# Optimization experiments

Hardware: AMD Instinct MI355X
Metric: run time of the kernel (lower is better)

Reference implementation:

```python
import jax, jax.numpy as jnp
import numpy as np

N_NODES = 8192
IN_FEAT = 128
OUT_FEAT = 64
N_EDGES = 262144


def gcn_conv(x, edge_index, W, b):
    # x: [N, F_in], edge_index: [2, E], W: [F_in, F_out], b: [F_out]
    n = x.shape[0]
    loop = jnp.arange(n, dtype=edge_index.dtype)
    src = jnp.concatenate([edge_index[0], loop])  # message sources (incl. self loops)
    dst = jnp.concatenate([edge_index[1], loop])  # aggregation targets
    # symmetric normalization D^{-1/2} (A+I) D^{-1/2}
    deg = jax.ops.segment_sum(jnp.ones_like(dst, dtype=x.dtype), dst, num_segments=n)
    dinv = jax.lax.rsqrt(jnp.where(deg > 0, deg, 1.0))
    norm = dinv[src] * dinv[dst]  # [E + N]
    h = x @ W  # [N, F_out]
    out = jax.ops.segment_sum(h[src] * norm[:, None], dst, num_segments=n)
    return out + b


def setup_inputs() -> dict:
    key = jax.random.key(0)
    k1, k2, k3, k4 = jax.random.split(key, 4)
    x = jax.random.normal(k1, (IN_FEAT, N_NODES), dtype=jnp.float32)
    edge_index = jax.random.randint(k2, (2, N_EDGES), 0, N_NODES, dtype=jnp.int64)
    # encoder GCNConv params (glorot-ish scale)
    W_enc = jax.random.normal(k3, (IN_FEAT, OUT_FEAT), dtype=jnp.float32) / np.sqrt(IN_FEAT)
    b_enc = jnp.zeros((OUT_FEAT,), dtype=jnp.float32)
    return {"x": x, "edge_index": edge_index, "W_enc": W_enc, "b_enc": b_enc}


def reference(x, edge_index, W_enc, b_enc):
    xt = x.T  # [N, F_in]
    z = gcn_conv(xt, edge_index, W_enc, b_enc)  # [N, F_out]
    adj_pred = jax.nn.sigmoid(z @ z.T)  # [N, N]
    return adj_pred
```

## Files before the change

### kernel.cpp

```cpp
#include <hip/hip_runtime.h>
#include <hip/hip_bf16.h>

#define N_NODES 8192
#define F_IN    128
#define F_OUT   64
#define N_EDGES 262144

typedef unsigned int   u32;
typedef unsigned short u16;
typedef __attribute__((ext_vector_type(8))) short short8;
typedef __attribute__((ext_vector_type(4))) float f32x4;

__device__ __forceinline__ u16 f2bf_rne(float f) {
    u32 u = __float_as_uint(f);
    u32 r = (u + 0x7FFFu + ((u >> 16) & 1u)) >> 16;
    return (u16)r;
}
__device__ __forceinline__ float bf2f(u16 b) {
    return __uint_as_float(((u32)b) << 16);
}

__global__ __launch_bounds__(256) void detect_kernel(const int* __restrict__ ei,
                                                     const u32* __restrict__ xw,
                                                     int* __restrict__ eflag,
                                                     int* __restrict__ xdt) {
    if (blockIdx.x < 32) {
        int i = blockIdx.x * 256 + threadIdx.x;
        if (ei[2 * i + 1] != 0) atomicOr(eflag, 1);
    } else {
        __shared__ int cnt;
        if (threadIdx.x == 0) cnt = 0;
        __syncthreads();
        u32 w = xw[threadIdx.x * 64 + 1];
        u32 e = (w >> 7) & 0xFFu;
        if (e >= 100u && e <= 134u) atomicAdd(&cnt, 1);
        __syncthreads();
        if (threadIdx.x == 0) *xdt = (cnt > 128) ? 1 : 0;
    }
}

__global__ __launch_bounds__(256) void deg_kernel(const int* __restrict__ ei,
                                                  const int* __restrict__ eflagp,
                                                  int* __restrict__ deg) {
    int e = blockIdx.x * 256 + threadIdx.x;
    bool is64 = (*eflagp == 0);
    int d = is64 ? ei[2 * (N_EDGES + e)] : ei[N_EDGES + e];
    atomicAdd(&deg[d], 1);
}

__global__ __launch_bounds__(1024) void scan_kernel(const int* __restrict__ deg,
                                                    int* __restrict__ offs,
                                                    int* __restrict__ cursor) {
    __shared__ int part[1024];
    int t = threadIdx.x;
    int loc[8];
    int run = 0;
    #pragma unroll
    for (int j = 0; j < 8; ++j) { loc[j] = run; run += deg[t * 8 + j]; }
    part[t] = run;
    __syncthreads();
    for (int d = 1; d < 1024; d <<= 1) {
        int v = (t >= d) ? part[t - d] : 0;
        __syncthreads();
        part[t] += v;
        __syncthreads();
    }
    int pre = part[t] - run;
    #pragma unroll
    for (int j = 0; j < 8; ++j) {
        int v = pre + loc[j];
        offs[t * 8 + j]   = v;
        cursor[t * 8 + j] = v;
    }
    if (t == 1023) offs[8192] = pre + run;
}

__global__ __launch_bounds__(256) void fill_feat_kernel(
        const int* __restrict__ ei, const int* __restrict__ eflagp,
        int* __restrict__ cursor, int* __restrict__ esrc,
        const void* __restrict__ xv, const void* __restrict__ Wv,
        const void* __restrict__ bv, const int* __restrict__ xdtp,
        const int* __restrict__ deg,
        float* __restrict__ dinv,
        float* __restrict__ h,
        float* __restrict__ z)
{
    __shared__ float Wl[F_IN * F_OUT];
    int t = threadIdx.x;

    if (blockIdx.x < N_EDGES / 256) {
        int e = blockIdx.x * 256 + t;
        bool is64 = (*eflagp == 0);
        int s = is64 ? ei[2 * e]             : ei[e];
        int d = is64 ? ei[2 * (N_EDGES + e)] : ei[N_EDGES + e];
        int pos = atomicAdd(&cursor[d], 1);
        esrc[pos] = s;
        return;
    }

    const bool isbf = (*xdtp != 0);
    if (isbf) {
        const __hip_bfloat16* Wb = (const __hip_bfloat16*)Wv;
        for (int i = t; i < F_IN * F_OUT; i += 256) Wl[i] = (float)Wb[i];
    } else {
        const float* Wf = (const float*)Wv;
        for (int i = t; i < F_IN * F_OUT; i += 256) Wl[i] = Wf[i];
    }
    __syncthreads();

    int id = (blockIdx.x - N_EDGES / 256) * 256 + t;
    int og = id >> 13;
    int n  = id & (N_NODES - 1);

    float dv = rsqrtf((float)(deg[n] + 1));
    float acc[8] = {0.f,0.f,0.f,0.f,0.f,0.f,0.f,0.f};

    if (isbf) {
        const __hip_bfloat16* xb = (const __hip_bfloat16*)xv;
        for (int f = 0; f < F_IN; ++f) {
            float xval = (float)xb[f * N_NODES + n];
            const float4* w4 = (const float4*)&Wl[f * F_OUT + og * 8];
            float4 w0 = w4[0], w1 = w4[1];
            acc[0] += xval * w0.x; acc[1] += xval * w0.y;
            acc[2] += xval * w0.z; acc[3] += xval * w0.w;
            acc[4] += xval * w1.x; acc[5] += xval * w1.y;
            acc[6] += xval * w1.z; acc[7] += xval * w1.w;
        }
    } else {
        const float* xf = (const float*)xv;
        for (int f = 0; f < F_IN; ++f) {
            float xval = xf[f * N_NODES + n];
            const float4* w4 = (const float4*)&Wl[f * F_OUT + og * 8];
            float4 w0 = w4[0], w1 = w4[1];
            acc[0] += xval * w0.x; acc[1] += xval * w0.y;
            acc[2] += xval * w0.z; acc[3] += xval * w0.w;
            acc[4] += xval * w1.x; acc[5] += xval * w1.y;
            acc[6] += xval * w1.z; acc[7] += xval * w1.w;
        }
    }

    if (og == 0) dinv[n] = dv;

    float bvals[8];
    if (isbf) {
        const __hip_bfloat16* bb = (const __hip_bfloat16*)bv;
        #pragma unroll
        for (int j = 0; j < 8; ++j) bvals[j] = (float)bb[og * 8 + j];
    } else {
        const float* bf = (const float*)bv;
        #pragma unroll
        for (int j = 0; j < 8; ++j) bvals[j] = bf[og * 8 + j];
    }
    float hs[8], zb[8];
    #pragma unroll
    for (int j = 0; j < 8; ++j) {
        hs[j] = dv * acc[j];
        zb[j] = bvals[j] + dv * hs[j];
    }
    float* hp = h + (size_t)n * 64 + og * 8;
    ((float4*)hp)[0] = make_float4(hs[0], hs[1], hs[2], hs[3]);
    ((float4*)hp)[1] = make_float4(hs[4], hs[5], hs[6], hs[7]);
    float* zp = z + (size_t)n * 64 + og * 8;
    ((float4*)zp)[0] = make_float4(zb[0], zb[1], zb[2], zb[3]);
    ((float4*)zp)[1] = make_float4(zb[4], zb[5], zb[6], zb[7]);
}

__global__ __launch_bounds__(256) void gather_kernel(
        const int* __restrict__ offs, const int* __restrict__ esrc,
        const float* __restrict__ h, const float* __restrict__ dinv,
        float* __restrict__ z)
{
    int t = blockIdx.x * 256 + threadIdx.x;
    int d = t >> 6;
    int o = t & 63;
    int beg = offs[d], end = offs[d + 1];
    float acc = 0.f;
    for (int i = beg; i < end; ++i) {
        int s = esrc[i];
        acc += h[(size_t)s * 64 + o];
    }
    z[(size_t)d * 64 + o] += dinv[d] * acc;
}

__global__ __launch_bounds__(256) void gemm_sig_kernel(
        const float* __restrict__ z, float* __restrict__ out)
{
    __shared__ __align__(16) char smem[128 * 129 * 4];
    u16 (*Ah)[64] = (u16(*)[64])(smem);
    u16 (*Al)[64] = (u16(*)[64])(smem + 16384);
    u16 (*Bh)[64] = (u16(*)[64])(smem + 32768);
    u16 (*Bl)[64] = (u16(*)[64])(smem + 49152);
    float (*Cs)[129] = (float(*)[129])(smem);

    int t = threadIdx.x;

    int tgt = blockIdx.x;
    int bi = (int)((sqrtf(8.f * (float)tgt + 1.f) - 1.f) * 0.5f);
    while ((bi + 1) * (bi + 2) / 2 <= tgt) ++bi;
    while (bi * (bi + 1) / 2 > tgt) --bi;
    int bj = tgt - bi * (bi + 1) / 2;
    int i0 = bi * 128;
    int j0 = bj * 128;
    bool offdiag = (bi != bj);

    #pragma unroll
    for (int it = 0; it < 8; ++it) {
        int item = it * 256 + t;
        int tile = item >> 10;
        int r    = (item >> 3) & 127;
        int c    = item & 7;
        const float* src = z + (size_t)((tile ? j0 : i0) + r) * 64 + c * 8;
        float4 v0 = ((const float4*)src)[0];
        float4 v1 = ((const float4*)src)[1];
        float vf[8] = {v0.x, v0.y, v0.z, v0.w, v1.x, v1.y, v1.z, v1.w};
        short8 sh, sl;
        #pragma unroll
        for (int j = 0; j < 8; ++j) {
            float f  = vf[j];
            u16 hb   = f2bf_rne(f);
            u16 lb   = f2bf_rne(f - bf2f(hb));
            sh[j] = (short)hb;
            sl[j] = (short)lb;
        }
        int cs = c ^ (r & 7);
        u16* dh = tile ? &Bh[r][cs * 8] : &Ah[r][cs * 8];
        u16* dl = tile ? &Bl[r][cs * 8] : &Al[r][cs * 8];
        *(short8*)dh = sh;
        *(short8*)dl = sl;
    }
    __syncthreads();

    int lane = t & 63;
    int w    = t >> 6;
    int lr   = lane & 15;
    int lk   = lane >> 4;

    short8 ah[2][2], al[2][2];
    #pragma unroll
    for (int rt = 0; rt < 2; ++rt)
        #pragma unroll
        for (int kh = 0; kh < 2; ++kh) {
            int rl = w * 32 + rt * 16 + lr;
            int cs = (kh * 4 + lk) ^ (rl & 7);
            ah[rt][kh] = *(const short8*)&Ah[rl][cs * 8];
            al[rt][kh] = *(const short8*)&Al[rl][cs * 8];
        }

    f32x4 acc[2][8];
    #pragma unroll
    for (int rt = 0; rt < 2; ++rt)
        #pragma unroll
        for (int ct = 0; ct < 8; ++ct)
            acc[rt][ct] = (f32x4){0.f, 0.f, 0.f, 0.f};

    #pragma unroll
    for (int ct = 0; ct < 8; ++ct) {
        short8 bh[2], bl[2];
        #pragma unroll
        for (int kh = 0; kh < 2; ++kh) {
            int rl = ct * 16 + lr;
            int cs = (kh * 4 + lk) ^ (rl & 7);
            bh[kh] = *(const short8*)&Bh[rl][cs * 8];
            bl[kh] = *(const short8*)&Bl[rl][cs * 8];
        }
        #pragma unroll
        for (int rt = 0; rt < 2; ++rt) {
            #pragma unroll
            for (int kh = 0; kh < 2; ++kh) {
                acc[rt][ct] = __builtin_amdgcn_mfma_f32_16x16x32_bf16(
                    ah[rt][kh], bh[kh], acc[rt][ct], 0, 0, 0);
                acc[rt][ct] = __builtin_amdgcn_mfma_f32_16x16x32_bf16(
                    ah[rt][kh], bl[kh], acc[rt][ct], 0, 0, 0);
                acc[rt][ct] = __builtin_amdgcn_mfma_f32_16x16x32_bf16(
                    al[rt][kh], bh[kh], acc[rt][ct], 0, 0, 0);
            }
        }
    }

    #pragma unroll
    for (int rt = 0; rt < 2; ++rt)
        #pragma unroll
        for (int ct = 0; ct < 8; ++ct)
            #pragma unroll
            for (int rg = 0; rg < 4; ++rg) {
                float v = acc[rt][ct][rg];
                acc[rt][ct][rg] =
                    __builtin_amdgcn_rcpf(1.f + __expf(-v));
            }

    if (offdiag) {
        __syncthreads();
        #pragma unroll
        for (int rt = 0; rt < 2; ++rt)
            #pragma unroll
            for (int ct = 0; ct < 8; ++ct) {
                int col = ct * 16 + lr;
                int row = w * 32 + rt * 16 + lk * 4;
                #pragma unroll
                for (int rg = 0; rg < 4; ++rg)
                    Cs[row + rg][col] = acc[rt][ct][rg];
            }
    }

    #pragma unroll
    for (int rt = 0; rt < 2; ++rt)
        #pragma unroll
        for (int ct = 0; ct < 8; ++ct) {
            int gcol = j0 + ct * 16 + lr;
            #pragma unroll
            for (int rg = 0; rg < 4; ++rg) {
                int grow = i0 + w * 32 + rt * 16 + lk * 4 + rg;
                out[(size_t)grow * N_NODES + gcol] = acc[rt][ct][rg];
            }
        }

    if (offdiag) {
        __syncthreads();
        #pragma unroll
        for (int u = 0; u < 16; ++u) {
            int q   = u * 256 + t;
            int rr  = q >> 5;
            int cc4 = (q & 31) * 4;
            float4 v = make_float4(Cs[cc4 + 0][rr], Cs[cc4 + 1][rr],
                                   Cs[cc4 + 2][rr], Cs[cc4 + 3][rr]);
            *(float4*)(out + (size_t)(j0 + rr) * N_NODES + i0 + cc4) = v;
        }
    }
}

extern "C" void kernel_launch(void* const* d_in, const int* in_sizes, int n_in,
                              void* d_out, int out_size, void* d_ws, size_t ws_size,
                              hipStream_t stream) {
    const void* x  = d_in[0];
    const int*  ei = (const int*)d_in[1];
    const void* W  = d_in[2];
    const void* b  = d_in[3];
    float* out = (float*)d_out;

    char* ws = (char*)d_ws;
    int*   deg    = (int*)ws;
    int*   eflag  = (int*)(ws + 32768);
    int*   xdt    = (int*)(ws + 32784);
    int*   offs   = (int*)(ws + 36864);
    int*   cursor = (int*)(ws + 73728);
    float* dinv   = (float*)(ws + 110592);
    int*   esrc   = (int*)(ws + 147456);
    float* h      = (float*)(ws + 1196032);
    float* z      = (float*)(ws + 3293184);

    hipMemsetAsync(ws, 0, 36864, stream);
    detect_kernel<<<33, 256, 0, stream>>>(ei, (const u32*)x, eflag, xdt);
    deg_kernel<<<N_EDGES / 256, 256, 0, stream>>>(ei, eflag, deg);
    scan_kernel<<<1, 1024, 0, stream>>>(deg, offs, cursor);
    fill_feat_kernel<<<N_EDGES / 256 + 256, 256, 0, stream>>>(
        ei, eflag, cursor, esrc, x, W, b, xdt, deg, dinv, h, z);
    gather_kernel<<<N_NODES * 64 / 256, 256, 0, stream>>>(offs, esrc, h, dinv, z);
    gemm_sig_kernel<<<64 * 65 / 2, 256, 0, stream>>>(z, out);
}
```

Baseline: 344.2 us.

## Pre-split z into packed bf16 hi/lo and load GEMM tiles via global_load_lds

The gather kernel now writes z as packed bf16 hi/lo pairs, so the GEMM loads tiles straight into LDS with global_load_lds and unpacks them with perm instructions instead of converting fp32 per block. Output stores become nontemporal, to avoid polluting cache with the 256MB result. The feature kernel computes 16 outputs per thread with half the blocks, and degree zeroing moves into an init kernel, replacing a larger memset. The output write bandwidth still dominates, so gains are limited to the tile load, conversion and launch overhead.

Result: slower. 362.6 us (+5.3%).

```diff
diff --git a/kernel.cpp b/kernel.cpp
--- a/kernel.cpp
+++ b/kernel.cpp
@@ -10,6 +10,11 @@
 typedef unsigned short u16;
 typedef __attribute__((ext_vector_type(8))) short short8;
 typedef __attribute__((ext_vector_type(4))) float f32x4;
+typedef __attribute__((ext_vector_type(4))) u32 u32x4;
+
+__device__ __forceinline__ int SWZ(int r) {
+    return (((r) & 3) << 1) | (((r) >> 2) & 1);
+}
 
 __device__ __forceinline__ u16 f2bf_rne(float f) {
     u32 u = __float_as_uint(f);
@@ -20,14 +25,15 @@
     return __uint_as_float(((u32)b) << 16);
 }
 
-__global__ __launch_bounds__(256) void detect_kernel(const int* __restrict__ ei,
-                                                     const u32* __restrict__ xw,
-                                                     int* __restrict__ eflag,
-                                                     int* __restrict__ xdt) {
+__global__ __launch_bounds__(256) void init_kernel(const int* __restrict__ ei,
+                                                   const u32* __restrict__ xw,
+                                                   int* __restrict__ eflag,
+                                                   int* __restrict__ xdt,
+                                                   int* __restrict__ deg) {
     if (blockIdx.x < 32) {
         int i = blockIdx.x * 256 + threadIdx.x;
         if (ei[2 * i + 1] != 0) atomicOr(eflag, 1);
-    } else {
+    } else if (blockIdx.x == 32) {
         __shared__ int cnt;
         if (threadIdx.x == 0) cnt = 0;
         __syncthreads();
@@ -36,6 +42,9 @@
         if (e >= 100u && e <= 134u) atomicAdd(&cnt, 1);
         __syncthreads();
         if (threadIdx.x == 0) *xdt = (cnt > 128) ? 1 : 0;
+    } else {
+        int i = (blockIdx.x - 33) * 256 + threadIdx.x;
+        deg[i] = 0;
     }
 }
 
@@ -113,56 +122,61 @@
     int n  = id & (N_NODES - 1);
 
     float dv = rsqrtf((float)(deg[n] + 1));
-    float acc[8] = {0.f,0.f,0.f,0.f,0.f,0.f,0.f,0.f};
+    float acc[16];
+    #pragma unroll
+    for (int j = 0; j < 16; ++j) acc[j] = 0.f;
 
     if (isbf) {
         const __hip_bfloat16* xb = (const __hip_bfloat16*)xv;
         for (int f = 0; f < F_IN; ++f) {
             float xval = (float)xb[f * N_NODES + n];
-            const float4* w4 = (const float4*)&Wl[f * F_OUT + og * 8];
-            float4 w0 = w4[0], w1 = w4[1];
-            acc[0] += xval * w0.x; acc[1] += xval * w0.y;
-            acc[2] += xval * w0.z; acc[3] += xval * w0.w;
-            acc[4] += xval * w1.x; acc[5] += xval * w1.y;
-            acc[6] += xval * w1.z; acc[7] += xval * w1.w;
+            const float4* w4 = (const float4*)&Wl[f * F_OUT + og * 16];
+            #pragma unroll
+            for (int q = 0; q < 4; ++q) {
+                float4 wv = w4[q];
+                acc[q*4+0] += xval * wv.x; acc[q*4+1] += xval * wv.y;
+                acc[q*4+2] += xval * wv.z; acc[q*4+3] += xval * wv.w;
+            }
         }
     } else {
         const float* xf = (const float*)xv;
         for (int f = 0; f < F_IN; ++f) {
             float xval = xf[f * N_NODES + n];
-            const float4* w4 = (const float4*)&Wl[f * F_OUT + og * 8];
-            float4 w0 = w4[0], w1 = w4[1];
-            acc[0] += xval * w0.x; acc[1] += xval * w0.y;
-            acc[2] += xval * w0.z; acc[3] += xval * w0.w;
-            acc[4] += xval * w1.x; acc[5] += xval * w1.y;
-            acc[6] += xval * w1.z; acc[7] += xval * w1.w;
+            const float4* w4 = (const float4*)&Wl[f * F_OUT + og * 16];
+            #pragma unroll
+            for (int q = 0; q < 4; ++q) {
+                float4 wv = w4[q];
+                acc[q*4+0] += xval * wv.x; acc[q*4+1] += xval * wv.y;
+                acc[q*4+2] += xval * wv.z; acc[q*4+3] += xval * wv.w;
+            }
         }
     }
 
     if (og == 0) dinv[n] = dv;
 
-    float bvals[8];
+    float bvals[16];
     if (isbf) {
         const __hip_bfloat16* bb = (const __hip_bfloat16*)bv;
         #pragma unroll
-        for (int j = 0; j < 8; ++j) bvals[j] = (float)bb[og * 8 + j];
+        for (int j = 0; j < 16; ++j) bvals[j] = (float)bb[og * 16 + j];
     } else {
         const float* bf = (const float*)bv;
         #pragma unroll
-        for (int j = 0; j < 8; ++j) bvals[j] = bf[og * 8 + j];
-    }
-    float hs[8], zb[8];
-    #pragma unroll
-    for (int j = 0; j < 8; ++j) {
-        hs[j] = dv * acc[j];
-        zb[j] = bvals[j] + dv * hs[j];
-    }
-    float* hp = h + (size_t)n * 64 + og * 8;
-    ((float4*)hp)[0] = make_float4(hs[0], hs[1], hs[2], hs[3]);
-    ((float4*)hp)[1] = make_float4(hs[4], hs[5], hs[6], hs[7]);
-    float* zp = z + (size_t)n * 64 + og * 8;
-    ((float4*)zp)[0] = make_float4(zb[0], zb[1], zb[2], zb[3]);
-    ((float4*)zp)[1] = make_float4(zb[4], zb[5], zb[6], zb[7]);
+        for (int j = 0; j < 16; ++j) bvals[j] = bf[og * 16 + j];
+    }
+    float* hp = h + (size_t)n * 64 + og * 16;
+    float* zp = z + (size_t)n * 64 + og * 16;
+    #pragma unroll
+    for (int q = 0; q < 4; ++q) {
+        float hs[4], zb[4];
+        #pragma unroll
+        for (int j = 0; j < 4; ++j) {
+            hs[j] = dv * acc[q*4+j];
+            zb[j] = bvals[q*4+j] + dv * hs[j];
+        }
+        ((float4*)hp)[q] = make_float4(hs[0], hs[1], hs[2], hs[3]);
+        ((float4*)zp)[q] = make_float4(zb[0], zb[1], zb[2], zb[3]);
+    }
 }
 
 __global__ __launch_bounds__(256) void gather_kernel(
@@ -179,20 +193,23 @@
         int s = esrc[i];
         acc += h[(size_t)s * 64 + o];
     }
-    z[(size_t)d * 64 + o] += dinv[d] * acc;
+    float fin = z[(size_t)d * 64 + o] + dinv[d] * acc;
+    u16 hb = f2bf_rne(fin);
+    u16 lb = f2bf_rne(fin - bf2f(hb));
+    ((u32*)z)[(size_t)d * 64 + o] = ((u32)hb << 16) | (u32)lb;
 }
 
 __global__ __launch_bounds__(256) void gemm_sig_kernel(
-        const float* __restrict__ z, float* __restrict__ out)
+        const u32* __restrict__ zhl, float* __restrict__ out)
 {
-    __shared__ __align__(16) char smem[128 * 129 * 4];
-    u16 (*Ah)[64] = (u16(*)[64])(smem);
-    u16 (*Al)[64] = (u16(*)[64])(smem + 16384);
-    u16 (*Bh)[64] = (u16(*)[64])(smem + 32768);
-    u16 (*Bl)[64] = (u16(*)[64])(smem + 49152);
-    float (*Cs)[129] = (float(*)[129])(smem);
-
-    int t = threadIdx.x;
+    __shared__ __align__(16) u32 smem[128 * 129];
+    u32* Az = smem;
+    u32* Bz = smem + 8192;
+    float* Cs = (float*)smem;
+
+    int t    = threadIdx.x;
+    int lane = t & 63;
+    int w    = t >> 6;
 
     int tgt = blockIdx.x;
     int bi = (int)((sqrtf(8.f * (float)tgt + 1.f) - 1.f) * 0.5f);
@@ -204,36 +221,24 @@
     bool offdiag = (bi != bj);
 
     #pragma unroll
-    for (int it = 0; it < 8; ++it) {
-        int item = it * 256 + t;
-        int tile = item >> 10;
-        int r    = (item >> 3) & 127;
-        int c    = item & 7;
-        const float* src = z + (size_t)((tile ? j0 : i0) + r) * 64 + c * 8;
-        float4 v0 = ((const float4*)src)[0];
-        float4 v1 = ((const float4*)src)[1];
-        float vf[8] = {v0.x, v0.y, v0.z, v0.w, v1.x, v1.y, v1.z, v1.w};
-        short8 sh, sl;
-        #pragma unroll
-        for (int j = 0; j < 8; ++j) {
-            float f  = vf[j];
-            u16 hb   = f2bf_rne(f);
-            u16 lb   = f2bf_rne(f - bf2f(hb));
-            sh[j] = (short)hb;
-            sl[j] = (short)lb;
-        }
-        int cs = c ^ (r & 7);
-        u16* dh = tile ? &Bh[r][cs * 8] : &Ah[r][cs * 8];
-        u16* dl = tile ? &Bl[r][cs * 8] : &Al[r][cs * 8];
-        *(short8*)dh = sh;
-        *(short8*)dl = sl;
+    for (int T = 0; T < 2; ++T) {
+        int rbase = T ? j0 : i0;
+        u32* dstT = T ? Bz : Az;
+        #pragma unroll
+        for (int jj = 0; jj < 8; ++jj) {
+            int instr = w * 8 + jj;
+            int q  = instr * 64 + lane;
+            int r  = q >> 4;
+            int ch = q & 15;
+            int cs = ch ^ SWZ(r);
+            const u32* g = zhl + (size_t)(rbase + r) * 64 + cs * 4;
+            __builtin_amdgcn_global_load_lds(g, dstT + instr * 256, 16, 0, 0);
+        }
     }
     __syncthreads();
 
-    int lane = t & 63;
-    int w    = t >> 6;
-    int lr   = lane & 15;
-    int lk   = lane >> 4;
+    int lr = lane & 15;
+    int lk = lane >> 4;
 
     short8 ah[2][2], al[2][2];
     #pragma unroll
@@ -241,9 +246,18 @@
         #pragma unroll
         for (int kh = 0; kh < 2; ++kh) {
             int rl = w * 32 + rt * 16 + lr;
-            int cs = (kh * 4 + lk) ^ (rl & 7);
-            ah[rt][kh] = *(const short8*)&Ah[rl][cs * 8];
-            al[rt][kh] = *(const short8*)&Al[rl][cs * 8];
+            int c0 = (kh * 4 + lk) * 2;
+            u32x4 q0 = *(const u32x4*)&Az[rl * 64 + ((c0    ) ^ SWZ(rl)) * 4];
+            u32x4 q1 = *(const u32x4*)&Az[rl * 64 + ((c0 + 1) ^ SWZ(rl)) * 4];
+            u32 v[8] = {q0.x, q0.y, q0.z, q0.w, q1.x, q1.y, q1.z, q1.w};
+            u32x4 hi, lo;
+            #pragma unroll
+            for (int j = 0; j < 4; ++j) {
+                hi[j] = __builtin_amdgcn_perm(v[2*j+1], v[2*j], 0x07060302u);
+                lo[j] = __builtin_amdgcn_perm(v[2*j+1], v[2*j], 0x05040100u);
+            }
+            ah[rt][kh] = __builtin_bit_cast(short8, hi);
+            al[rt][kh] = __builtin_bit_cast(short8, lo);
         }
 
     f32x4 acc[2][8];
@@ -259,9 +273,18 @@
         #pragma unroll
         for (int kh = 0; kh < 2; ++kh) {
             int rl = ct * 16 + lr;
-            int cs = (kh * 4 + lk) ^ (rl & 7);
-            bh[kh] = *(const short8*)&Bh[rl][cs * 8];
-            bl[kh] = *(const short8*)&Bl[rl][cs * 8];
+            int c0 = (kh * 4 + lk) * 2;
+            u32x4 q0 = *(const u32x4*)&Bz[rl * 64 + ((c0    ) ^ SWZ(rl)) * 4];
+            u32x4 q1 = *(const u32x4*)&Bz[rl * 64 + ((c0 + 1) ^ SWZ(rl)) * 4];
+            u32 v[8] = {q0.x, q0.y, q0.z, q0.w, q1.x, q1.y, q1.z, q1.w};
+            u32x4 hi, lo;
+            #pragma unroll
+            for (int j = 0; j < 4; ++j) {
+                hi[j] = __builtin_amdgcn_perm(v[2*j+1], v[2*j], 0x07060302u);
+                lo[j] = __builtin_amdgcn_perm(v[2*j+1], v[2*j], 0x05040100u);
+            }
+            bh[kh] = __builtin_bit_cast(short8, hi);
+            bl[kh] = __builtin_bit_cast(short8, lo);
         }
         #pragma unroll
         for (int rt = 0; rt < 2; ++rt) {
@@ -284,8 +307,7 @@
             #pragma unroll
             for (int rg = 0; rg < 4; ++rg) {
                 float v = acc[rt][ct][rg];
-                acc[rt][ct][rg] =
-                    __builtin_amdgcn_rcpf(1.f + __expf(-v));
+                acc[rt][ct][rg] = __builtin_amdgcn_rcpf(1.f + __expf(-v));
             }
 
     if (offdiag) {
@@ -298,7 +320,7 @@
                 int row = w * 32 + rt * 16 + lk * 4;
                 #pragma unroll
                 for (int rg = 0; rg < 4; ++rg)
-                    Cs[row + rg][col] = acc[rt][ct][rg];
+                    Cs[(row + rg) * 129 + col] = acc[rt][ct][rg];
             }
     }
 
@@ -310,7 +332,8 @@
             #pragma unroll
             for (int rg = 0; rg < 4; ++rg) {
                 int grow = i0 + w * 32 + rt * 16 + lk * 4 + rg;
-                out[(size_t)grow * N_NODES + gcol] = acc[rt][ct][rg];
+                __builtin_nontemporal_store(acc[rt][ct][rg],
+                    out + (size_t)grow * N_NODES + gcol);
             }
         }
 
@@ -321,9 +344,13 @@
             int q   = u * 256 + t;
             int rr  = q >> 5;
             int cc4 = (q & 31) * 4;
-            float4 v = make_float4(Cs[cc4 + 0][rr], Cs[cc4 + 1][rr],
-                                   Cs[cc4 + 2][rr], Cs[cc4 + 3][rr]);
-            *(float4*)(out + (size_t)(j0 + rr) * N_NODES + i0 + cc4) = v;
+            f32x4 v;
+            v[0] = Cs[(cc4 + 0) * 129 + rr];
+            v[1] = Cs[(cc4 + 1) * 129 + rr];
+            v[2] = Cs[(cc4 + 2) * 129 + rr];
+            v[3] = Cs[(cc4 + 3) * 129 + rr];
+            __builtin_nontemporal_store(v,
+                (f32x4*)(out + (size_t)(j0 + rr) * N_NODES + i0 + cc4));
         }
     }
 }
@@ -348,12 +375,12 @@
     float* h      = (float*)(ws + 1196032);
     float* z      = (float*)(ws + 3293184);
 
-    hipMemsetAsync(ws, 0, 36864, stream);
-    detect_kernel<<<33, 256, 0, stream>>>(ei, (const u32*)x, eflag, xdt);
+    (void)hipMemsetAsync(ws + 32768, 0, 32, stream);
+    init_kernel<<<65, 256, 0, stream>>>(ei, (const u32*)x, eflag, xdt, deg);
     deg_kernel<<<N_EDGES / 256, 256, 0, stream>>>(ei, eflag, deg);
     scan_kernel<<<1, 1024, 0, stream>>>(deg, offs, cursor);
-    fill_feat_kernel<<<N_EDGES / 256 + 256, 256, 0, stream>>>(
+    fill_feat_kernel<<<N_EDGES / 256 + 128, 256, 0, stream>>>(
         ei, eflag, cursor, esrc, x, W, b, xdt, deg, dinv, h, z);
     gather_kernel<<<N_NODES * 64 / 256, 256, 0, stream>>>(offs, esrc, h, dinv, z);
-    gemm_sig_kernel<<<64 * 65 / 2, 256, 0, stream>>>(z, out);
-}
+    gemm_sig_kernel<<<64 * 65 / 2, 256, 0, stream>>>((const u32*)z, out);
+}
```
